# Kernel optimization log

Hardware: AMD Instinct MI355X
Metric: run time of the kernel (lower is better)

## Reference

```python
import jax, jax.numpy as jnp
import numpy as np

BASE_R = 0.1      # base_radius (compared against squared distances)
K = 20            # PositionEncoder k
H = 0.1           # dilated_ball_query bandwidth
EPS_BN = 1e-5


def _gelu(x):
    return jax.nn.gelu(x, approximate=False)  # torch nn.GELU default (erf)


def _bn(x, g, b):
    # eval-mode BatchNorm (running_mean=0, running_var=1), channel axis = 1
    shape = (1, -1) + (1,) * (x.ndim - 2)
    scale = g / np.float32(np.sqrt(1.0 + EPS_BN))
    return x * scale.reshape(shape) + b.reshape(shape)


def _conv1x1(x, w):
    # pointwise conv (no bias): w [out_c, in_c], x [B, in_c, ...]
    return jnp.einsum('oc,bc...->bo...', w, x)


def _l1norm(x, axis):
    # F.normalize(p=1): divide by L1 norm clamped to 1e-12
    return x / jnp.maximum(jnp.sum(jnp.abs(x), axis=axis, keepdims=True), 1e-12)


def _forward(xyz, w_q, g_q, b_q, w_k, g_k, b_k, w_v, g_v, b_v,
             w_pe, b_pe, g_pe, bb_pe, w_m1, g_m1, b_m1, w_m2, g_m2, b_m2,
             w_out, g_out, b_out):
    B, _, N = xyz.shape
    # ---- pairwise squared distances [B,N,N] ----
    sq = jnp.sum(xyz * xyz, axis=1)
    dist = -2.0 * jnp.einsum('bcn,bcm->bnm', xyz, xyz) + sq[:, :, None] + sq[:, None, :]
    # ---- dilated ball query (sigma=1) ----
    gauss = jnp.exp(-dist / (2.0 * H * H))
    kd = jnp.sum(gauss, axis=-1, keepdims=True)                 # [B,N,1]
    kd_score = kd / (jnp.max(kd, axis=1, keepdims=True) + 1e-9)
    radius = BASE_R + BASE_R * kd_score                         # max_radius = 2*base
    keep = dist < radius                                        # [B,N,N]
    # ---- masked attention (emb_cent == emb_x == cat(xyz, xyz)) ----
    emb = jnp.concatenate([xyz, xyz], axis=1)                   # [B,6,N]
    q = _bn(_conv1x1(emb, w_q), g_q, b_q)                       # [B,1,N]
    k_ = _bn(_conv1x1(emb, w_k), g_k, b_k)                      # [B,1,N]
    scores = jnp.einsum('bhn,bhm->bnm', q, k_)                  # [B,N,N]
    scores = jnp.where(keep, scores, -1e9)
    adj = jax.nn.softmax(scores, axis=-1)
    adj = _l1norm(_l1norm(adj, 1), -1)                          # doubly L1-normalized
    # ---- graph smoothing + value conv ----
    smoothed = jnp.einsum('bcn,bnm->bcm', xyz, adj)
    variation = smoothed - xyz
    v = _bn(_conv1x1(jnp.concatenate([variation, xyz], axis=1), w_v), g_v, b_v)  # [B,64,N]
    # ---- position encoder: ball-query top-k neighbor gather ----
    ar = jnp.arange(N, dtype=jnp.int32)[None, None, :]
    idx = jnp.where(dist > radius, N, ar)                       # mark out-of-ball with N
    idx = jnp.sort(idx, axis=-1)[:, :, :K]                      # k nearest-index in-ball
    idx = jnp.where(idx == N, idx[:, :, :1], idx)               # pad with first neighbor
    grouped = jax.vmap(lambda f, i: f[:, i])(xyz, idx)          # [B,3,N,K]
    pts = jnp.broadcast_to(xyz[:, :, :, None], grouped.shape)
    pf = jnp.concatenate([pts, grouped, grouped - pts], axis=1)  # [B,9,N,K]
    pf = _conv1x1(pf, w_pe) + b_pe[None, :, None, None]          # conv2d 1x1 with bias
    pf = _gelu(_bn(pf, g_pe, bb_pe))
    pf = jnp.max(pf, axis=-1)                                    # [B,out/8,N]
    pf = _gelu(_bn(_conv1x1(pf, w_m1), g_m1, b_m1))              # [B,out/4,N]
    pos = _bn(_conv1x1(pf, w_m2), g_m2, b_m2)                    # [B,out,N]
    out = _gelu(v + pos)
    return _bn(_conv1x1(out, w_out), g_out, b_out)               # [B,32,N]


def setup_inputs() -> dict:
    key = jax.random.key(0)
    ks = iter(jax.random.split(key, 40))
    B, N, OC = 4, 4096, 64

    def w(shape):
        return jax.random.normal(next(ks), shape, jnp.float32) / np.float32(np.sqrt(shape[-1]))

    def gb(c):
        g = 1.0 + 0.1 * jax.random.normal(next(ks), (c,), jnp.float32)
        b = 0.1 * jax.random.normal(next(ks), (c,), jnp.float32)
        return g, b

    xyz = jax.random.uniform(next(ks), (B, 3, N), jnp.float32)
    g_q, b_q = gb(1)
    g_k, b_k = gb(1)
    g_v, b_v = gb(OC)
    g_pe, bb_pe = gb(OC // 8)
    g_m1, b_m1 = gb(OC // 4)
    g_m2, b_m2 = gb(OC)
    g_out, b_out = gb(32)
    return {
        'xyz': xyz,
        'w_q': w((1, 6)), 'g_q': g_q, 'b_q': b_q,
        'w_k': w((1, 6)), 'g_k': g_k, 'b_k': b_k,
        'w_v': w((OC, 6)), 'g_v': g_v, 'b_v': b_v,
        'w_pe': w((OC // 8, 9)), 'b_pe': 0.1 * jax.random.normal(next(ks), (OC // 8,), jnp.float32),
        'g_pe': g_pe, 'bb_pe': bb_pe,
        'w_m1': w((OC // 4, OC // 8)), 'g_m1': g_m1, 'b_m1': b_m1,
        'w_m2': w((OC, OC // 4)), 'g_m2': g_m2, 'b_m2': b_m2,
        'w_out': w((32, OC)), 'g_out': g_out, 'b_out': b_out,
    }


def reference(xyz, w_q, g_q, b_q, w_k, g_k, b_k, w_v, g_v, b_v,
              w_pe, b_pe, g_pe, bb_pe, w_m1, g_m1, b_m1, w_m2, g_m2, b_m2,
              w_out, g_out, b_out):
    return _forward(xyz, w_q, g_q, b_q, w_k, g_k, b_k, w_v, g_v, b_v,
                    w_pe, b_pe, g_pe, bb_pe, w_m1, g_m1, b_m1, w_m2, g_m2, b_m2,
                    w_out, g_out, b_out)
```

## Files before the change

### kernel.cpp

```cpp
#include <hip/hip_runtime.h>
#include <math.h>

#define BB 4
#define NN 4096
#define KNBR 20
#define BN (BB * NN)
#define HALF 2048
#define RPW 128

__device__ __forceinline__ float gelu_f(float x) {
    return 0.5f * x * (1.0f + erff(x * 0.70710678118654752440f));
}

__global__ void k0_prep(const float* __restrict__ xyz,
                        const float* __restrict__ w_q, const float* __restrict__ g_q, const float* __restrict__ b_q,
                        const float* __restrict__ w_k, const float* __restrict__ g_k, const float* __restrict__ b_k,
                        float* __restrict__ qv, float* __restrict__ kv, float4* __restrict__ pts4) {
    int t = blockIdx.x * blockDim.x + threadIdx.x;
    if (t >= BN) return;
    int b = t / NN, n = t % NN;
    const float* base = xyz + (size_t)b * 3 * NN;
    float x = base[n], y = base[NN + n], z = base[2 * NN + n];
    float sq = x * x + y * y + z * z;
    const float invs = rsqrtf(1.0f + 1e-5f);
    float qr = x * (w_q[0] + w_q[3]) + y * (w_q[1] + w_q[4]) + z * (w_q[2] + w_q[5]);
    float kr = x * (w_k[0] + w_k[3]) + y * (w_k[1] + w_k[4]) + z * (w_k[2] + w_k[5]);
    qv[t] = qr * (g_q[0] * invs) + b_q[0];
    kv[t] = kr * (g_k[0] * invs) + b_k[0];
    pts4[t] = make_float4(x, y, z, sq);
}


__global__ __launch_bounds__(1024, 8)
void p1_kd(const float4* __restrict__ pts4, float* __restrict__ part) {
    int tid = threadIdx.x;
    int wave = __builtin_amdgcn_readfirstlane(tid >> 6);
    int lane = tid & 63;
    int g = blockIdx.x >> 1, half = blockIdx.x & 1;
    int out = g * 64 + lane;
    int b = g >> 6;
    const float4* p = pts4 + (size_t)b * NN;
    float4 fr = pts4[out];
    float acc = 0.f;
    int i0 = half * HALF + wave * RPW;
    #pragma unroll 4
    for (int i = i0; i < i0 + RPW; ++i) {
        float4 fc = p[i];
        float dot = fr.x * fc.x + fr.y * fc.y + fr.z * fc.z;
        float d = fmaf(-2.0f, dot, fr.w) + fc.w;
        acc += __expf(-50.0f * d);
    }
    __shared__ float s_red[16][64];
    s_red[wave][lane] = acc;
    __syncthreads();
    if (tid < 64) {
        float s = 0.f;
        #pragma unroll
        for (int w = 0; w < 16; ++w) s += s_red[w][tid];
        part[half * BN + g * 64 + tid] = s;
    }
}

__global__ void k2_radius(const float* __restrict__ part, float* __restrict__ radius) {
    int b = blockIdx.x;
    int t = threadIdx.x;
    float kdv[4];
    float mx = -1e30f;
    #pragma unroll
    for (int j = 0; j < 4; ++j) {
        int n = b * NN + j * 1024 + t;
        kdv[j] = part[n] + part[BN + n];
        mx = fmaxf(mx, kdv[j]);
    }
    __shared__ float red[1024];
    red[t] = mx;
    __syncthreads();
    for (int s = 512; s > 0; s >>= 1) {
        if (t < s) red[t] = fmaxf(red[t], red[t + s]);
        __syncthreads();
    }
    float kmax = red[0];
    #pragma unroll
    for (int j = 0; j < 4; ++j) {
        int n = b * NN + j * 1024 + t;
        radius[n] = 0.1f + 0.1f * (kdv[j] / (kmax + 1e-9f));
    }
}

__global__ __launch_bounds__(1024, 8)
void p3_Z(const float4* __restrict__ pts4, const float* __restrict__ qv,
          const float* __restrict__ kv, const float* __restrict__ radius,
          float* __restrict__ part) {
    int tid = threadIdx.x;
    int wave = __builtin_amdgcn_readfirstlane(tid >> 6);
    int lane = tid & 63;
    int g = blockIdx.x >> 1, half = blockIdx.x & 1;
    int row = g * 64 + lane;
    int b = g >> 6;
    const float4* p = pts4 + (size_t)b * NN;
    const float* kb = kv + (size_t)b * NN;
    float4 fr = pts4[row];
    float qn = qv[row], rad = radius[row];
    float acc = 0.f;
    int i0 = half * HALF + wave * RPW;
    #pragma unroll 4
    for (int i = i0; i < i0 + RPW; ++i) {
        float4 fc = p[i];
        float dot = fr.x * fc.x + fr.y * fc.y + fr.z * fc.z;
        float d = fmaf(-2.0f, dot, fr.w) + fc.w;
        float e = __expf(qn * kb[i]);
        acc += (d < rad) ? e : 0.f;
    }
    __shared__ float s_red[16][64];
    s_red[wave][lane] = acc;
    __syncthreads();
    if (tid < 64) {
        float s = 0.f;
        #pragma unroll
        for (int w = 0; w < 16; ++w) s += s_red[w][tid];
        part[half * BN + g * 64 + tid] = s;
    }
}

__global__ void r3_Z(const float* __restrict__ part, const float* __restrict__ qv,
                     const float* __restrict__ radius, float* __restrict__ Z,
                     float4* __restrict__ aux_a) {
    int t = blockIdx.x * blockDim.x + threadIdx.x;
    float s = part[t] + part[BN + t];
    Z[t] = s;
    aux_a[t] = make_float4(qv[t], radius[t], __logf(s), 0.f);
}

__global__ __launch_bounds__(1024, 8)
void p4_colsum(const float4* __restrict__ pts4, const float4* __restrict__ aux_a,
               const float* __restrict__ kv, float* __restrict__ part) {
    int tid = threadIdx.x;
    int wave = __builtin_amdgcn_readfirstlane(tid >> 6);
    int lane = tid & 63;
    int g = blockIdx.x >> 1, half = blockIdx.x & 1;
    int col = g * 64 + lane;
    int b = g >> 6;
    const float4* p = pts4 + (size_t)b * NN;
    const float4* a = aux_a + (size_t)b * NN;
    float4 fcc = pts4[col];
    float km = kv[col];
    float acc = 0.f;
    int i0 = half * HALF + wave * RPW;
    #pragma unroll 4
    for (int i = i0; i < i0 + RPW; ++i) {
        float4 fr = p[i];
        float4 an = a[i];
        float dot = fr.x * fcc.x + fr.y * fcc.y + fr.z * fcc.z;
        float d = fmaf(-2.0f, dot, fr.w) + fcc.w;
        float e = __expf(an.x * km - an.z);
        acc += (d < an.y) ? e : 0.f;
    }
    __shared__ float s_red[16][64];
    s_red[wave][lane] = acc;
    __syncthreads();
    if (tid < 64) {
        float s = 0.f;
        #pragma unroll
        for (int w = 0; w < 16; ++w) s += s_red[w][tid];
        part[half * BN + g * 64 + tid] = s;
    }
}

__global__ void r4_colsum(const float* __restrict__ part, const float* __restrict__ kv,
                          float* __restrict__ colsum, float2* __restrict__ kc2) {
    int t = blockIdx.x * blockDim.x + threadIdx.x;
    float s = fmaxf(part[t] + part[BN + t], 1e-12f);
    colsum[t] = s;
    kc2[t] = make_float2(kv[t], __logf(s));
}

__global__ __launch_bounds__(1024, 8)
void p5_rs(const float4* __restrict__ pts4, const float* __restrict__ qv,
           const float* __restrict__ radius, const float2* __restrict__ kc2,
           float* __restrict__ part) {
    int tid = threadIdx.x;
    int wave = __builtin_amdgcn_readfirstlane(tid >> 6);
    int lane = tid & 63;
    int g = blockIdx.x >> 1, half = blockIdx.x & 1;
    int row = g * 64 + lane;
    int b = g >> 6;
    const float4* p = pts4 + (size_t)b * NN;
    const float2* kc = kc2 + (size_t)b * NN;
    float4 fr = pts4[row];
    float qn = qv[row], rad = radius[row];
    float acc = 0.f;
    int i0 = half * HALF + wave * RPW;
    #pragma unroll 4
    for (int i = i0; i < i0 + RPW; ++i) {
        float4 fc = p[i];
        float2 km = kc[i];
        float dot = fr.x * fc.x + fr.y * fc.y + fr.z * fc.z;
        float d = fmaf(-2.0f, dot, fr.w) + fc.w;
        float e = __expf(qn * km.x - km.y);
        acc += (d < rad) ? e : 0.f;
    }
    __shared__ float s_red[16][64];
    s_red[wave][lane] = acc;
    __syncthreads();
    if (tid < 64) {
        float s = 0.f;
        #pragma unroll
        for (int w = 0; w < 16; ++w) s += s_red[w][tid];
        part[half * BN + g * 64 + tid] = s;
    }
}

__global__ void r5_rs(const float* __restrict__ part, const float* __restrict__ Z,
                      float4* __restrict__ aux_a) {
    int t = blockIdx.x * blockDim.x + threadIdx.x;
    float s = part[t] + part[BN + t];
    float rs = fmaxf(s / Z[t], 1e-12f);
    float4 a = aux_a[t];
    a.w = a.z + __logf(rs);
    aux_a[t] = a;
}

__global__ __launch_bounds__(1024, 8)
void p6_smooth(const float4* __restrict__ pts4, const float4* __restrict__ aux_a,
               const float* __restrict__ kv, float* __restrict__ partx,
               float* __restrict__ party, float* __restrict__ partz) {
    int tid = threadIdx.x;
    int wave = __builtin_amdgcn_readfirstlane(tid >> 6);
    int lane = tid & 63;
    int g = blockIdx.x >> 1, half = blockIdx.x & 1;
    int col = g * 64 + lane;
    int b = g >> 6;
    const float4* p = pts4 + (size_t)b * NN;
    const float4* a = aux_a + (size_t)b * NN;
    float4 fcc = pts4[col];
    float km = kv[col];
    float ax = 0.f, ay = 0.f, az = 0.f;
    int i0 = half * HALF + wave * RPW;
    #pragma unroll 4
    for (int i = i0; i < i0 + RPW; ++i) {
        float4 fr = p[i];
        float4 an = a[i];
        float dot = fr.x * fcc.x + fr.y * fcc.y + fr.z * fcc.z;
        float d = fmaf(-2.0f, dot, fr.w) + fcc.w;
        float w = __expf(an.x * km - an.w);
        w = (d < an.y) ? w : 0.f;
        ax += fr.x * w;
        ay += fr.y * w;
        az += fr.z * w;
    }
    __shared__ float s_rx[16][64];
    __shared__ float s_ry[16][64];
    __shared__ float s_rz[16][64];
    s_rx[wave][lane] = ax;
    s_ry[wave][lane] = ay;
    s_rz[wave][lane] = az;
    __syncthreads();
    if (tid < 64) {
        float sx = 0.f, sy = 0.f, sz = 0.f;
        #pragma unroll
        for (int w = 0; w < 16; ++w) {
            sx += s_rx[w][tid];
            sy += s_ry[w][tid];
            sz += s_rz[w][tid];
        }
        int o = half * BN + g * 64 + tid;
        partx[o] = sx;
        party[o] = sy;
        partz[o] = sz;
    }
}

__global__ void k7_pe_idx(const float4* __restrict__ pts4, const float* __restrict__ radius,
                          int* __restrict__ idxg) {
    int wave = threadIdx.x >> 6, lane = threadIdx.x & 63;
    int row = blockIdx.x * 4 + wave;
    int b = row / NN;
    const float4* p = pts4 + (size_t)b * NN;
    float4 fr = pts4[row];
    float rad = radius[row];
    int total = 0;
    int firstm = 0;
    bool have = false;
    unsigned long long lmask = (1ULL << lane) - 1ULL;
    for (int i = 0; i < NN / 64 && total < KNBR; ++i) {
        int m = i * 64 + lane;
        float4 fc = p[m];
        float dot = fr.x * fc.x + fr.y * fc.y + fr.z * fc.z;
        float d = fmaf(-2.0f, dot, fr.w) + fc.w;
        bool inb = !(d > rad);
        unsigned long long mask = __ballot(inb);
        if (!have && mask != 0ULL) {
            int src = __ffsll(mask) - 1;
            firstm = __shfl(m, src);
            have = true;
        }
        int pos = total + (int)__popcll(mask & lmask);
        if (inb && pos < KNBR) idxg[(size_t)row * KNBR + pos] = m;
        total += (int)__popcll(mask);
    }
    if (total < KNBR && lane >= total && lane < KNBR)
        idxg[(size_t)row * KNBR + lane] = firstm;
}

__global__ void k8_final(const float* __restrict__ xyz,
                         const float* __restrict__ partx, const float* __restrict__ party,
                         const float* __restrict__ partz, const float* __restrict__ colsum,
                         const int* __restrict__ idxg,
                         const float* __restrict__ w_v, const float* __restrict__ g_v, const float* __restrict__ b_v,
                         const float* __restrict__ w_pe, const float* __restrict__ b_pe,
                         const float* __restrict__ g_pe, const float* __restrict__ bb_pe,
                         const float* __restrict__ w_m1, const float* __restrict__ g_m1, const float* __restrict__ b_m1,
                         const float* __restrict__ w_m2, const float* __restrict__ g_m2, const float* __restrict__ b_m2,
                         const float* __restrict__ w_out, const float* __restrict__ g_out, const float* __restrict__ b_out,
                         float* __restrict__ out) {
    __shared__ float s_pf8[32][9];
    __shared__ float s_pf16[32][17];
    __shared__ float s_g64[32][65];
    int tid = threadIdx.x;
    int ptL = tid >> 3, o = tid & 7;
    int p = blockIdx.x * 32 + ptL;
    int b = p / NN, n = p % NN;
    const float* xb = xyz + (size_t)b * 3 * NN;
    float x = xb[n], y = xb[NN + n], z = xb[2 * NN + n];
    const float invs = rsqrtf(1.0f + 1e-5f);

    float w0 = w_pe[o * 9 + 0], w1 = w_pe[o * 9 + 1], w2 = w_pe[o * 9 + 2];
    float w3 = w_pe[o * 9 + 3], w4 = w_pe[o * 9 + 4], w5 = w_pe[o * 9 + 5];
    float w6 = w_pe[o * 9 + 6], w7 = w_pe[o * 9 + 7], w8 = w_pe[o * 9 + 8];
    float bp = b_pe[o], gp = g_pe[o] * invs, bbp = bb_pe[o];
    float mx = -1e30f;
    for (int kk = 0; kk < KNBR; ++kk) {
        int j = idxg[(size_t)p * KNBR + kk];
        float gx = xb[j], gy = xb[NN + j], gz = xb[2 * NN + j];
        float dx = gx - x, dy = gy - y, dz = gz - z;
        float s = w0 * x + w1 * y + w2 * z + w3 * gx + w4 * gy + w5 * gz
                + w6 * dx + w7 * dy + w8 * dz + bp;
        s = gelu_f(s * gp + bbp);
        mx = fmaxf(mx, s);
    }
    s_pf8[ptL][o] = mx;
    __syncthreads();

    #pragma unroll
    for (int rr = 0; rr < 2; ++rr) {
        int r = o + rr * 8;
        const float* w = w_m1 + r * 8;
        float s = 0.f;
        #pragma unroll
        for (int c = 0; c < 8; ++c) s += w[c] * s_pf8[ptL][c];
        s_pf16[ptL][r] = gelu_f(s * (g_m1[r] * invs) + b_m1[r]);
    }
    __syncthreads();

    float inv = 1.0f / colsum[p];
    float vx = (partx[p] + partx[BN + p]) * inv - x;
    float vy = (party[p] + party[BN + p]) * inv - y;
    float vz = (partz[p] + partz[BN + p]) * inv - z;
    #pragma unroll
    for (int i = 0; i < 8; ++i) {
        int ch = o * 8 + i;
        const float* wm = w_m2 + ch * 16;
        float pos = 0.f;
        #pragma unroll
        for (int c = 0; c < 16; ++c) pos += wm[c] * s_pf16[ptL][c];
        pos = pos * (g_m2[ch] * invs) + b_m2[ch];
        const float* wv = w_v + ch * 6;
        float vv = wv[0] * vx + wv[1] * vy + wv[2] * vz + wv[3] * x + wv[4] * y + wv[5] * z;
        vv = vv * (g_v[ch] * invs) + b_v[ch];
        s_g64[ptL][ch] = gelu_f(vv + pos);
    }
    __syncthreads();

    #pragma unroll
    for (int i = 0; i < 4; ++i) {
        int ch = o * 4 + i;
        const float* w = w_out + ch * 64;
        float s = 0.f;
        #pragma unroll
        for (int c = 0; c < 64; ++c) s += w[c] * s_g64[ptL][c];
        out[((size_t)b * 32 + ch) * NN + n] = s * (g_out[ch] * invs) + b_out[ch];
    }
}

extern "C" void kernel_launch(void* const* d_in, const int* in_sizes, int n_in,
                              void* d_out, int out_size, void* d_ws, size_t ws_size,
                              hipStream_t stream) {
    const float* xyz  = (const float*)d_in[0];
    const float* w_q  = (const float*)d_in[1];
    const float* g_q  = (const float*)d_in[2];
    const float* b_q  = (const float*)d_in[3];
    const float* w_k  = (const float*)d_in[4];
    const float* g_k  = (const float*)d_in[5];
    const float* b_k  = (const float*)d_in[6];
    const float* w_v  = (const float*)d_in[7];
    const float* g_v  = (const float*)d_in[8];
    const float* b_v  = (const float*)d_in[9];
    const float* w_pe = (const float*)d_in[10];
    const float* b_pe = (const float*)d_in[11];
    const float* g_pe = (const float*)d_in[12];
    const float* bb_pe= (const float*)d_in[13];
    const float* w_m1 = (const float*)d_in[14];
    const float* g_m1 = (const float*)d_in[15];
    const float* b_m1 = (const float*)d_in[16];
    const float* w_m2 = (const float*)d_in[17];
    const float* g_m2 = (const float*)d_in[18];
    const float* b_m2 = (const float*)d_in[19];
    const float* w_out= (const float*)d_in[20];
    const float* g_out= (const float*)d_in[21];
    const float* b_out= (const float*)d_in[22];

    float* ws = (float*)d_ws;
    float*  qv       = ws;
    float*  kv       = ws + (size_t)1 * BN;
    float4* pts4     = (float4*)(ws + (size_t)2 * BN);
    float*  radius   = ws + (size_t)6 * BN;
    float*  Zv       = ws + (size_t)7 * BN;
    float*  colsum   = ws + (size_t)8 * BN;
    float4* aux_a    = (float4*)(ws + (size_t)9 * BN);
    float2* kc2      = (float2*)(ws + (size_t)13 * BN);
    int*    idxg     = (int*)(ws + (size_t)15 * BN);
    float*  part_s   = ws + (size_t)35 * BN;
    float*  partx    = ws + (size_t)37 * BN;
    float*  party    = ws + (size_t)39 * BN;
    float*  partz    = ws + (size_t)41 * BN;

    const int PB = (BN / 64) * 2;

    k0_prep<<<BN / 256, 256, 0, stream>>>(xyz, w_q, g_q, b_q, w_k, g_k, b_k, qv, kv, pts4);
    p1_kd<<<PB, 1024, 0, stream>>>(pts4, part_s);
    k2_radius<<<BB, 1024, 0, stream>>>(part_s, radius);
    p3_Z<<<PB, 1024, 0, stream>>>(pts4, qv, kv, radius, part_s);
    r3_Z<<<BN / 256, 256, 0, stream>>>(part_s, qv, radius, Zv, aux_a);
    p4_colsum<<<PB, 1024, 0, stream>>>(pts4, aux_a, kv, part_s);
    r4_colsum<<<BN / 256, 256, 0, stream>>>(part_s, kv, colsum, kc2);
    p5_rs<<<PB, 1024, 0, stream>>>(pts4, qv, radius, kc2, part_s);
    r5_rs<<<BN / 256, 256, 0, stream>>>(part_s, Zv, aux_a);
    p6_smooth<<<PB, 1024, 0, stream>>>(pts4, aux_a, kv, partx, party, partz);
    k7_pe_idx<<<BN / 4, 256, 0, stream>>>(pts4, radius, idxg);
    k8_final<<<BN / 32, 256, 0, stream>>>(xyz, partx, party, partz, colsum, idxg,
                                          w_v, g_v, b_v,
                                          w_pe, b_pe, g_pe, bb_pe,
                                          w_m1, g_m1, b_m1,
                                          w_m2, g_m2, b_m2,
                                          w_out, g_out, b_out,
                                          (float*)d_out);
}
```

Baseline: 277.3 us.

## Interleave per-point records, batch-unroll pair loops, fold neighbor search into Z pass

Packs point coordinates and per-point scalars into interleaved 32-byte records (recB..recE), so each pair-loop iteration reads one contiguous record pair instead of separate arrays. It also unrolls all pairwise loops by 8 with the loads grouped ahead of the math, and fuses the k-neighbor index search into the tail of the Z pass, which removes one kernel launch. The cost is extra record-building writes in the small reduction kernels, a larger workspace, and more register pressure under the 1024x8 launch bounds.

```diff
diff --git a/kernel.cpp b/kernel.cpp
--- a/kernel.cpp
+++ b/kernel.cpp
@@ -30,25 +30,27 @@
     pts4[t] = make_float4(x, y, z, sq);
 }
 
-
 __global__ __launch_bounds__(1024, 8)
 void p1_kd(const float4* __restrict__ pts4, float* __restrict__ part) {
     int tid = threadIdx.x;
     int wave = __builtin_amdgcn_readfirstlane(tid >> 6);
     int lane = tid & 63;
     int g = blockIdx.x >> 1, half = blockIdx.x & 1;
-    int out = g * 64 + lane;
     int b = g >> 6;
     const float4* p = pts4 + (size_t)b * NN;
-    float4 fr = pts4[out];
+    float4 fr = pts4[g * 64 + lane];
     float acc = 0.f;
     int i0 = half * HALF + wave * RPW;
-    #pragma unroll 4
-    for (int i = i0; i < i0 + RPW; ++i) {
-        float4 fc = p[i];
-        float dot = fr.x * fc.x + fr.y * fc.y + fr.z * fc.z;
-        float d = fmaf(-2.0f, dot, fr.w) + fc.w;
-        acc += __expf(-50.0f * d);
+    for (int i = i0; i < i0 + RPW; i += 8) {
+        float4 fc[8];
+        #pragma unroll
+        for (int u = 0; u < 8; ++u) fc[u] = p[i + u];
+        #pragma unroll
+        for (int u = 0; u < 8; ++u) {
+            float dot = fr.x * fc[u].x + fr.y * fc[u].y + fr.z * fc[u].z;
+            float d = fmaf(-2.0f, dot, fr.w) + fc[u].w;
+            acc += __expf(-50.0f * d);
+        }
     }
     __shared__ float s_red[16][64];
     s_red[wave][lane] = acc;
@@ -61,7 +63,9 @@
     }
 }
 
-__global__ void k2_radius(const float* __restrict__ part, float* __restrict__ radius) {
+__global__ void k2_radius(const float* __restrict__ part, const float4* __restrict__ pts4,
+                          const float* __restrict__ qv, const float* __restrict__ kv,
+                          float* __restrict__ radius, float4* __restrict__ recB) {
     int b = blockIdx.x;
     int t = threadIdx.x;
     float kdv[4];
@@ -83,33 +87,43 @@
     #pragma unroll
     for (int j = 0; j < 4; ++j) {
         int n = b * NN + j * 1024 + t;
-        radius[n] = 0.1f + 0.1f * (kdv[j] / (kmax + 1e-9f));
+        float rad = 0.1f + 0.1f * (kdv[j] / (kmax + 1e-9f));
+        radius[n] = rad;
+        recB[2 * n] = pts4[n];
+        recB[2 * n + 1] = make_float4(kv[n], qv[n], rad, 0.f);
     }
 }
 
 __global__ __launch_bounds__(1024, 8)
-void p3_Z(const float4* __restrict__ pts4, const float* __restrict__ qv,
-          const float* __restrict__ kv, const float* __restrict__ radius,
-          float* __restrict__ part) {
+void p3_Zk7(const float4* __restrict__ recB, const float4* __restrict__ pts4,
+            const float* __restrict__ radius, float* __restrict__ part,
+            int* __restrict__ idxg) {
     int tid = threadIdx.x;
     int wave = __builtin_amdgcn_readfirstlane(tid >> 6);
     int lane = tid & 63;
     int g = blockIdx.x >> 1, half = blockIdx.x & 1;
+    int b = g >> 6;
+    const float4* rb = recB + (size_t)b * NN * 2;
     int row = g * 64 + lane;
-    int b = g >> 6;
-    const float4* p = pts4 + (size_t)b * NN;
-    const float* kb = kv + (size_t)b * NN;
-    float4 fr = pts4[row];
-    float qn = qv[row], rad = radius[row];
+    float4 fr = recB[2 * row];
+    float4 rowa = recB[2 * row + 1];
+    float qn = rowa.y, rad = rowa.z;
     float acc = 0.f;
     int i0 = half * HALF + wave * RPW;
-    #pragma unroll 4
-    for (int i = i0; i < i0 + RPW; ++i) {
-        float4 fc = p[i];
-        float dot = fr.x * fc.x + fr.y * fc.y + fr.z * fc.z;
-        float d = fmaf(-2.0f, dot, fr.w) + fc.w;
-        float e = __expf(qn * kb[i]);
-        acc += (d < rad) ? e : 0.f;
+    for (int i = i0; i < i0 + RPW; i += 8) {
+        float4 fc[8], an[8];
+        #pragma unroll
+        for (int u = 0; u < 8; ++u) {
+            fc[u] = rb[2 * (i + u)];
+            an[u] = rb[2 * (i + u) + 1];
+        }
+        #pragma unroll
+        for (int u = 0; u < 8; ++u) {
+            float dot = fr.x * fc[u].x + fr.y * fc[u].y + fr.z * fc[u].z;
+            float d = fmaf(-2.0f, dot, fr.w) + fc[u].w;
+            float e = __expf(qn * an[u].x);
+            acc += (d < rad) ? e : 0.f;
+        }
     }
     __shared__ float s_red[16][64];
     s_red[wave][lane] = acc;
@@ -120,40 +134,75 @@
         for (int w = 0; w < 16; ++w) s += s_red[w][tid];
         part[half * BN + g * 64 + tid] = s;
     }
-}
-
-__global__ void r3_Z(const float* __restrict__ part, const float* __restrict__ qv,
-                     const float* __restrict__ radius, float* __restrict__ Z,
-                     float4* __restrict__ aux_a) {
+    int gw = blockIdx.x * 16 + wave;
+    for (int rr = 0; rr < 2; ++rr) {
+        int row7 = gw * 2 + rr;
+        int b7 = row7 / NN;
+        const float4* p7 = pts4 + (size_t)b7 * NN;
+        float4 f7 = pts4[row7];
+        float rad7 = radius[row7];
+        int total = 0, firstm = 0;
+        bool have = false;
+        unsigned long long lmask = (1ULL << lane) - 1ULL;
+        for (int i = 0; i < NN / 64 && total < KNBR; ++i) {
+            int m = i * 64 + lane;
+            float4 fc = p7[m];
+            float dot = f7.x * fc.x + f7.y * fc.y + f7.z * fc.z;
+            float d = fmaf(-2.0f, dot, f7.w) + fc.w;
+            bool inb = !(d > rad7);
+            unsigned long long mask = __ballot(inb);
+            if (!have && mask != 0ULL) {
+                int src = __ffsll(mask) - 1;
+                firstm = __shfl(m, src);
+                have = true;
+            }
+            int pos = total + (int)__popcll(mask & lmask);
+            if (inb && pos < KNBR) idxg[(size_t)row7 * KNBR + pos] = m;
+            total += (int)__popcll(mask);
+        }
+        if (total < KNBR && lane >= total && lane < KNBR)
+            idxg[(size_t)row7 * KNBR + lane] = firstm;
+    }
+}
+
+__global__ void r3_Z(const float* __restrict__ part, const float4* __restrict__ pts4,
+                     const float* __restrict__ qv, const float* __restrict__ radius,
+                     float* __restrict__ Z, float4* __restrict__ recC) {
     int t = blockIdx.x * blockDim.x + threadIdx.x;
     float s = part[t] + part[BN + t];
     Z[t] = s;
-    aux_a[t] = make_float4(qv[t], radius[t], __logf(s), 0.f);
+    recC[2 * t] = pts4[t];
+    recC[2 * t + 1] = make_float4(qv[t], radius[t], __logf(s), 0.f);
 }
 
 __global__ __launch_bounds__(1024, 8)
-void p4_colsum(const float4* __restrict__ pts4, const float4* __restrict__ aux_a,
-               const float* __restrict__ kv, float* __restrict__ part) {
+void p4_colsum(const float4* __restrict__ recC, const float4* __restrict__ recB,
+               float* __restrict__ part) {
     int tid = threadIdx.x;
     int wave = __builtin_amdgcn_readfirstlane(tid >> 6);
     int lane = tid & 63;
     int g = blockIdx.x >> 1, half = blockIdx.x & 1;
+    int b = g >> 6;
+    const float4* rc = recC + (size_t)b * NN * 2;
     int col = g * 64 + lane;
-    int b = g >> 6;
-    const float4* p = pts4 + (size_t)b * NN;
-    const float4* a = aux_a + (size_t)b * NN;
-    float4 fcc = pts4[col];
-    float km = kv[col];
+    float4 fcc = recB[2 * col];
+    float km = recB[2 * col + 1].x;
     float acc = 0.f;
     int i0 = half * HALF + wave * RPW;
-    #pragma unroll 4
-    for (int i = i0; i < i0 + RPW; ++i) {
-        float4 fr = p[i];
-        float4 an = a[i];
-        float dot = fr.x * fcc.x + fr.y * fcc.y + fr.z * fcc.z;
-        float d = fmaf(-2.0f, dot, fr.w) + fcc.w;
-        float e = __expf(an.x * km - an.z);
-        acc += (d < an.y) ? e : 0.f;
+    for (int i = i0; i < i0 + RPW; i += 8) {
+        float4 fr[8], an[8];
+        #pragma unroll
+        for (int u = 0; u < 8; ++u) {
+            fr[u] = rc[2 * (i + u)];
+            an[u] = rc[2 * (i + u) + 1];
+        }
+        #pragma unroll
+        for (int u = 0; u < 8; ++u) {
+            float dot = fr[u].x * fcc.x + fr[u].y * fcc.y + fr[u].z * fcc.z;
+            float d = fmaf(-2.0f, dot, fr[u].w) + fcc.w;
+            float e = __expf(an[u].x * km - an[u].z);
+            acc += (d < an[u].y) ? e : 0.f;
+        }
     }
     __shared__ float s_red[16][64];
     s_red[wave][lane] = acc;
@@ -166,38 +215,45 @@
     }
 }
 
-__global__ void r4_colsum(const float* __restrict__ part, const float* __restrict__ kv,
-                          float* __restrict__ colsum, float2* __restrict__ kc2) {
+__global__ void r4_colsum(const float* __restrict__ part, const float4* __restrict__ pts4,
+                          const float* __restrict__ kv, float* __restrict__ colsum,
+                          float4* __restrict__ recD) {
     int t = blockIdx.x * blockDim.x + threadIdx.x;
     float s = fmaxf(part[t] + part[BN + t], 1e-12f);
     colsum[t] = s;
-    kc2[t] = make_float2(kv[t], __logf(s));
+    recD[2 * t] = pts4[t];
+    recD[2 * t + 1] = make_float4(kv[t], __logf(s), 0.f, 0.f);
 }
 
 __global__ __launch_bounds__(1024, 8)
-void p5_rs(const float4* __restrict__ pts4, const float* __restrict__ qv,
-           const float* __restrict__ radius, const float2* __restrict__ kc2,
+void p5_rs(const float4* __restrict__ recD, const float4* __restrict__ recB,
            float* __restrict__ part) {
     int tid = threadIdx.x;
     int wave = __builtin_amdgcn_readfirstlane(tid >> 6);
     int lane = tid & 63;
     int g = blockIdx.x >> 1, half = blockIdx.x & 1;
+    int b = g >> 6;
+    const float4* rd = recD + (size_t)b * NN * 2;
     int row = g * 64 + lane;
-    int b = g >> 6;
-    const float4* p = pts4 + (size_t)b * NN;
-    const float2* kc = kc2 + (size_t)b * NN;
-    float4 fr = pts4[row];
-    float qn = qv[row], rad = radius[row];
+    float4 fr = recB[2 * row];
+    float4 rowa = recB[2 * row + 1];
+    float qn = rowa.y, rad = rowa.z;
     float acc = 0.f;
     int i0 = half * HALF + wave * RPW;
-    #pragma unroll 4
-    for (int i = i0; i < i0 + RPW; ++i) {
-        float4 fc = p[i];
-        float2 km = kc[i];
-        float dot = fr.x * fc.x + fr.y * fc.y + fr.z * fc.z;
-        float d = fmaf(-2.0f, dot, fr.w) + fc.w;
-        float e = __expf(qn * km.x - km.y);
-        acc += (d < rad) ? e : 0.f;
+    for (int i = i0; i < i0 + RPW; i += 8) {
+        float4 fc[8], an[8];
+        #pragma unroll
+        for (int u = 0; u < 8; ++u) {
+            fc[u] = rd[2 * (i + u)];
+            an[u] = rd[2 * (i + u) + 1];
+        }
+        #pragma unroll
+        for (int u = 0; u < 8; ++u) {
+            float dot = fr.x * fc[u].x + fr.y * fc[u].y + fr.z * fc[u].z;
+            float d = fmaf(-2.0f, dot, fr.w) + fc[u].w;
+            float e = __expf(qn * an[u].x - an[u].y);
+            acc += (d < rad) ? e : 0.f;
+        }
     }
     __shared__ float s_red[16][64];
     s_red[wave][lane] = acc;
@@ -211,42 +267,48 @@
 }
 
 __global__ void r5_rs(const float* __restrict__ part, const float* __restrict__ Z,
-                      float4* __restrict__ aux_a) {
+                      const float4* __restrict__ recC, const float4* __restrict__ pts4,
+                      float4* __restrict__ recE) {
     int t = blockIdx.x * blockDim.x + threadIdx.x;
     float s = part[t] + part[BN + t];
     float rs = fmaxf(s / Z[t], 1e-12f);
-    float4 a = aux_a[t];
-    a.w = a.z + __logf(rs);
-    aux_a[t] = a;
+    float4 a = recC[2 * t + 1];
+    recE[2 * t] = pts4[t];
+    recE[2 * t + 1] = make_float4(a.x, a.y, a.z + __logf(rs), 0.f);
 }
 
 __global__ __launch_bounds__(1024, 8)
-void p6_smooth(const float4* __restrict__ pts4, const float4* __restrict__ aux_a,
-               const float* __restrict__ kv, float* __restrict__ partx,
-               float* __restrict__ party, float* __restrict__ partz) {
+void p6_smooth(const float4* __restrict__ recE, const float4* __restrict__ recB,
+               float* __restrict__ partx, float* __restrict__ party,
+               float* __restrict__ partz) {
     int tid = threadIdx.x;
     int wave = __builtin_amdgcn_readfirstlane(tid >> 6);
     int lane = tid & 63;
     int g = blockIdx.x >> 1, half = blockIdx.x & 1;
+    int b = g >> 6;
+    const float4* re = recE + (size_t)b * NN * 2;
     int col = g * 64 + lane;
-    int b = g >> 6;
-    const float4* p = pts4 + (size_t)b * NN;
-    const float4* a = aux_a + (size_t)b * NN;
-    float4 fcc = pts4[col];
-    float km = kv[col];
+    float4 fcc = recB[2 * col];
+    float km = recB[2 * col + 1].x;
     float ax = 0.f, ay = 0.f, az = 0.f;
     int i0 = half * HALF + wave * RPW;
-    #pragma unroll 4
-    for (int i = i0; i < i0 + RPW; ++i) {
-        float4 fr = p[i];
-        float4 an = a[i];
-        float dot = fr.x * fcc.x + fr.y * fcc.y + fr.z * fcc.z;
-        float d = fmaf(-2.0f, dot, fr.w) + fcc.w;
-        float w = __expf(an.x * km - an.w);
-        w = (d < an.y) ? w : 0.f;
-        ax += fr.x * w;
-        ay += fr.y * w;
-        az += fr.z * w;
+    for (int i = i0; i < i0 + RPW; i += 8) {
+        float4 fr[8], an[8];
+        #pragma unroll
+        for (int u = 0; u < 8; ++u) {
+            fr[u] = re[2 * (i + u)];
+            an[u] = re[2 * (i + u) + 1];
+        }
+        #pragma unroll
+        for (int u = 0; u < 8; ++u) {
+            float dot = fr[u].x * fcc.x + fr[u].y * fcc.y + fr[u].z * fcc.z;
+            float d = fmaf(-2.0f, dot, fr[u].w) + fcc.w;
+            float w = __expf(an[u].x * km - an[u].z);
+            w = (d < an[u].y) ? w : 0.f;
+            ax += fr[u].x * w;
+            ay += fr[u].y * w;
+            az += fr[u].z * w;
+        }
     }
     __shared__ float s_rx[16][64];
     __shared__ float s_ry[16][64];
@@ -268,38 +330,6 @@
         party[o] = sy;
         partz[o] = sz;
     }
-}
-
-__global__ void k7_pe_idx(const float4* __restrict__ pts4, const float* __restrict__ radius,
-                          int* __restrict__ idxg) {
-    int wave = threadIdx.x >> 6, lane = threadIdx.x & 63;
-    int row = blockIdx.x * 4 + wave;
-    int b = row / NN;
-    const float4* p = pts4 + (size_t)b * NN;
-    float4 fr = pts4[row];
-    float rad = radius[row];
-    int total = 0;
-    int firstm = 0;
-    bool have = false;
-    unsigned long long lmask = (1ULL << lane) - 1ULL;
-    for (int i = 0; i < NN / 64 && total < KNBR; ++i) {
-        int m = i * 64 + lane;
-        float4 fc = p[m];
-        float dot = fr.x * fc.x + fr.y * fc.y + fr.z * fc.z;
-        float d = fmaf(-2.0f, dot, fr.w) + fc.w;
-        bool inb = !(d > rad);
-        unsigned long long mask = __ballot(inb);
-        if (!have && mask != 0ULL) {
-            int src = __ffsll(mask) - 1;
-            firstm = __shfl(m, src);
-            have = true;
-        }
-        int pos = total + (int)__popcll(mask & lmask);
-        if (inb && pos < KNBR) idxg[(size_t)row * KNBR + pos] = m;
-        total += (int)__popcll(mask);
-    }
-    if (total < KNBR && lane >= total && lane < KNBR)
-        idxg[(size_t)row * KNBR + lane] = firstm;
 }
 
 __global__ void k8_final(const float* __restrict__ xyz,
@@ -410,33 +440,37 @@
     const float* b_out= (const float*)d_in[22];
 
     float* ws = (float*)d_ws;
-    float*  qv       = ws;
-    float*  kv       = ws + (size_t)1 * BN;
-    float4* pts4     = (float4*)(ws + (size_t)2 * BN);
-    float*  radius   = ws + (size_t)6 * BN;
-    float*  Zv       = ws + (size_t)7 * BN;
-    float*  colsum   = ws + (size_t)8 * BN;
-    float4* aux_a    = (float4*)(ws + (size_t)9 * BN);
-    float2* kc2      = (float2*)(ws + (size_t)13 * BN);
-    int*    idxg     = (int*)(ws + (size_t)15 * BN);
-    float*  part_s   = ws + (size_t)35 * BN;
-    float*  partx    = ws + (size_t)37 * BN;
-    float*  party    = ws + (size_t)39 * BN;
-    float*  partz    = ws + (size_t)41 * BN;
+    float*  qv     = ws;
+    float*  kv     = ws + (size_t)1  * BN;
+    float4* pts4   = (float4*)(ws + (size_t)2  * BN);
+    float*  radius = ws + (size_t)6  * BN;
+    float*  Zv     = ws + (size_t)7  * BN;
+    float*  colsum = ws + (size_t)8  * BN;
+    float4* recB   = (float4*)(ws + (size_t)9  * BN);
+    float4* recC   = (float4*)(ws + (size_t)17 * BN);
+    float4* recD   = (float4*)(ws + (size_t)25 * BN);
+    float4* recE   = (float4*)(ws + (size_t)33 * BN);
+    int*    idxg   = (int*)   (ws + (size_t)41 * BN);
+    float*  part1  = ws + (size_t)61 * BN;
+    float*  part3  = ws + (size_t)63 * BN;
+    float*  part5  = ws + (size_t)65 * BN;
+    float*  part7  = ws + (size_t)67 * BN;
+    float*  partx  = ws + (size_t)69 * BN;
+    float*  party  = ws + (size_t)71 * BN;
+    float*  partz  = ws + (size_t)73 * BN;
 
     const int PB = (BN / 64) * 2;
 
     k0_prep<<<BN / 256, 256, 0, stream>>>(xyz, w_q, g_q, b_q, w_k, g_k, b_k, qv, kv, pts4);
-    p1_kd<<<PB, 1024, 0, stream>>>(pts4, part_s);
-    k2_radius<<<BB, 1024, 0, stream>>>(part_s, radius);
-    p3_Z<<<PB, 1024, 0, stream>>>(pts4, qv, kv, radius, part_s);
-    r3_Z<<<BN / 256, 256, 0, stream>>>(part_s, qv, radius, Zv, aux_a);
-    p4_colsum<<<PB, 1024, 0, stream>>>(pts4, aux_a, kv, part_s);
-    r4_colsum<<<BN / 256, 256, 0, stream>>>(part_s, kv, colsum, kc2);
-    p5_rs<<<PB, 1024, 0, stream>>>(pts4, qv, radius, kc2, part_s);
-    r5_rs<<<BN / 256, 256, 0, stream>>>(part_s, Zv, aux_a);
-    p6_smooth<<<PB, 1024, 0, stream>>>(pts4, aux_a, kv, partx, party, partz);
-    k7_pe_idx<<<BN / 4, 256, 0, stream>>>(pts4, radius, idxg);
+    p1_kd<<<PB, 1024, 0, stream>>>(pts4, part1);
+    k2_radius<<<BB, 1024, 0, stream>>>(part1, pts4, qv, kv, radius, recB);
+    p3_Zk7<<<PB, 1024, 0, stream>>>(recB, pts4, radius, part3, idxg);
+    r3_Z<<<BN / 256, 256, 0, stream>>>(part3, pts4, qv, radius, Zv, recC);
+    p4_colsum<<<PB, 1024, 0, stream>>>(recC, recB, part5);
+    r4_colsum<<<BN / 256, 256, 0, stream>>>(part5, pts4, kv, colsum, recD);
+    p5_rs<<<PB, 1024, 0, stream>>>(recD, recB, part7);
+    r5_rs<<<BN / 256, 256, 0, stream>>>(part7, Zv, recC, pts4, recE);
+    p6_smooth<<<PB, 1024, 0, stream>>>(recE, recB, partx, party, partz);
     k8_final<<<BN / 32, 256, 0, stream>>>(xyz, partx, party, partz, colsum, idxg,
                                           w_v, g_v, b_v,
                                           w_pe, b_pe, g_pe, bb_pe,
```

After: 280.6 us. No clear change (+1.2%).
